# Optimization experiments

Hardware: AMD Instinct MI355X
Metric: run time of the kernel (lower is better)

The kernel has to match this reference:

```python
import jax, jax.numpy as jnp
import numpy as np

N = 256    # b_s == nq == h*q == h*v (forced by the module's reshape/matmul constraints)
A = 1024   # model dim 'a'
K_DIM = 1  # self.k (h*k must equal 1 for the .view to be valid)


def setup_inputs() -> dict:
    key = jax.random.key(0)
    ks = jax.random.split(key, 5)
    s = 0.02
    x = jax.random.normal(ks[0], (N, N, A), dtype=jnp.float32)
    Wq = jax.random.normal(ks[1], (N, A), dtype=jnp.float32) * s      # fc_q: a -> h*q = N
    bq = jnp.zeros((N,), dtype=jnp.float32)
    Wk = jax.random.normal(ks[2], (K_DIM, A), dtype=jnp.float32) * s  # fc_k: a -> h*k = 1
    bk = jnp.zeros((K_DIM,), dtype=jnp.float32)
    Wv = jax.random.normal(ks[3], (N, A), dtype=jnp.float32) * s      # fc_v: a -> h*v = N
    bv = jnp.zeros((N,), dtype=jnp.float32)
    Wo = jax.random.normal(ks[4], (A, N), dtype=jnp.float32) * s      # fc_o: h*v -> a
    bo = jnp.zeros((A,), dtype=jnp.float32)
    return {"x": x, "Wq": Wq, "bq": bq, "Wk": Wk, "bk": bk,
            "Wv": Wv, "bv": bv, "Wo": Wo, "bo": bo}


def reference(x, Wq, bq, Wk, bk, Wv, bv, Wo, bo):
    # q = fc_q(x): (b_s, nq, h*q)
    q = jnp.einsum('bna,qa->bnq', x, Wq) + bq
    # k = fc_k(x).view(b_s, nq).permute(1, 0): (nq, b_s)
    klin = (jnp.einsum('bna,ka->bnk', x, Wk) + bk)[..., 0]  # (b_s, nq)
    kT = klin.T                                             # (nq, b_s)
    # att = matmul(kT, q) / sqrt(self.k): 2D kT broadcast over batch of q
    att = jnp.einsum('nm,bmq->bnq', kT, q) / np.sqrt(np.float32(K_DIM))
    att = jax.nn.softmax(att, axis=-1)  # dropout = identity (eval mode)
    # v = fc_v(x): (b_s, nq, h*v)
    v = jnp.einsum('bna,va->bnv', x, Wv) + bv
    # out = matmul(v, att): batched (nq, h*v) @ (nq, h*q) with h*v == nq
    out = jnp.einsum('bnm,bmq->bnq', v, att)
    # fc_o: (..., h*v) -> (..., a)
    return jnp.einsum('bnv,av->bna', out, Wo) + bo
```

## Files before the change

kernel.cpp:

```cpp
#include <hip/hip_runtime.h>


typedef unsigned short u16;
typedef unsigned int   uint;
using f32x4  = __attribute__((ext_vector_type(4))) float;
using bf16x8 = __attribute__((ext_vector_type(8))) short;
using u16x4  = __attribute__((ext_vector_type(4))) u16;

#define DEVI static __device__ __forceinline__

DEVI u16 f2bf(float f){
  union { float f; uint u; } v; v.f = f;
  uint r = v.u + 0x7fffu + ((v.u >> 16) & 1u);
  return (u16)(r >> 16);
}
DEVI float bf2f(u16 h){
  union { uint u; float f; } v; v.u = ((uint)h) << 16;
  return v.f;
}

typedef const uint __attribute__((address_space(1)))* as1_cuintp;
typedef uint __attribute__((address_space(3)))* as3_uintp;

DEVI void gl_lds16(const void* g, void* l){
  __builtin_amdgcn_global_load_lds((as1_cuintp)g, (as3_uintp)l, 16, 0, 0);
}

template<int ROWS, int NW>
DEVI void stage_tile(const u16* __restrict__ g, long long rowStride,
                     u16* lds, int lane, int wave){
  constexpr int NLD = ROWS >> 3;
  #pragma unroll
  for (int j = 0; j < NLD/NW; ++j){
    int r0  = (wave + NW*j) << 3;
    int row = r0 + (lane >> 3);
    const u16* src = g + (long long)row * rowStride
                       + (((lane & 7) ^ (lane >> 3)) << 3);
    gl_lds16(src, lds + r0 * 64);
  }
}

DEVI bf16x8 ldfrag(const u16* s, int rbase, int kk, int lane){
  int row = rbase + (lane & 15);
  int c   = (kk << 2) + (lane >> 4);
  return *(const bf16x8*)(s + row*64 + ((c ^ (row & 7)) << 3));
}

__global__ __launch_bounds__(512, 2)
void k_qvkl(const float* __restrict__ x,
            const u16* __restrict__ Wqh, const u16* __restrict__ Wql,
            const u16* __restrict__ Wvh,
            const float* __restrict__ Wk, const float* __restrict__ bk,
            const float* __restrict__ bq, const float* __restrict__ bv,
            u16* __restrict__ qTh, u16* __restrict__ qTl,
            u16* __restrict__ vout,
            u16* __restrict__ klTh, u16* __restrict__ klTl)
{
  __shared__ __align__(16) u16 sX [128*64];
  __shared__ __align__(16) u16 sXl[128*64];
  __shared__ __align__(16) u16 sW [2][3*128*64];

  const int tid  = threadIdx.x;
  const int lane = tid & 63;
  const int wave = tid >> 6;
  const int wm   = wave >> 2;
  const int wn   = wave & 3;
  const int tileM = blockIdx.x << 7;

  f32x4 qacc[4][4], vacc[4][4];
  #pragma unroll
  for (int i=0;i<4;i++)
    #pragma unroll
    for (int j=0;j<4;j++){
      qacc[i][j][0]=0.f; qacc[i][j][1]=0.f; qacc[i][j][2]=0.f; qacc[i][j][3]=0.f;
      vacc[i][j][0]=0.f; vacc[i][j][1]=0.f; vacc[i][j][2]=0.f; vacc[i][j][3]=0.f;
    }
  float kacc[4] = {0.f, 0.f, 0.f, 0.f};

  stage_tile<128,8>(Wqh + 0, 1024, sW[0],         lane, wave);
  stage_tile<128,8>(Wql + 0, 1024, sW[0] + 8192,  lane, wave);
  stage_tile<128,8>(Wvh + 0, 1024, sW[0] + 16384, lane, wave);

  for (int kt = 0; kt < 1024; kt += 64){
    #pragma unroll
    for (int h = 0; h < 2; ++h){
      f32x4 xr[4];
      if (h == 0){
        #pragma unroll
        for (int j=0;j<4;j++){
          int f = tid + (j << 9);
          xr[j] = *(const f32x4*)(x + (long long)(tileM + (f >> 4))*1024
                                  + kt + ((f & 15) << 2));
        }
        __builtin_amdgcn_sched_barrier(0);
      }
      const bool last = (kt == 960) && (h == 1);
      if (!last){
        const int nh  = h ^ 1;
        const int nkt = (h == 0) ? kt : kt + 64;
        u16* wb = sW[h ^ 1];
        stage_tile<128,8>(Wqh + (nh << 7)*1024 + nkt, 1024, wb,         lane, wave);
        stage_tile<128,8>(Wql + (nh << 7)*1024 + nkt, 1024, wb + 8192,  lane, wave);
        stage_tile<128,8>(Wvh + (nh << 7)*1024 + nkt, 1024, wb + 16384, lane, wave);
      }
      if (h == 0){
        #pragma unroll
        for (int j=0;j<4;j++){
          int f   = tid + (j << 9);
          int row = f >> 4;
          int c16 = f & 15;
          f32x4 t = xr[j];
          u16x4 h4, l4;
          #pragma unroll
          for (int e=0;e<4;e++){
            u16 hh = f2bf(t[e]);
            h4[e] = hh;
            l4[e] = f2bf(t[e] - bf2f(hh));
          }
          int off = row*64 + (((c16 >> 1) ^ (row & 7)) << 3) + ((c16 & 1) << 2);
          *(u16x4*)(sX  + off) = h4;
          *(u16x4*)(sXl + off) = l4;
          f32x4 w = *(const f32x4*)(Wk + kt + (c16 << 2));
          kacc[j] += t[0]*w[0] + t[1]*w[1] + t[2]*w[2] + t[3]*w[3];
        }
      }
      if (!last) asm volatile("s_waitcnt vmcnt(6) lgkmcnt(0)" ::: "memory");
      else       asm volatile("s_waitcnt vmcnt(0) lgkmcnt(0)" ::: "memory");
      __builtin_amdgcn_s_barrier();
      __builtin_amdgcn_sched_barrier(0);

      {
        const u16* wb = sW[h];
        #pragma unroll
        for (int kk=0;kk<2;kk++){
          bf16x8 a[4], al[4];
          #pragma unroll
          for (int i=0;i<4;i++){
            a[i]  = ldfrag(sX , wm*64 + i*16, kk, lane);
            al[i] = ldfrag(sXl, wm*64 + i*16, kk, lane);
          }
          {
            bf16x8 b[2];
            #pragma unroll
            for (int i=0;i<2;i++) b[i] = ldfrag(wb, wn*32 + i*16, kk, lane);
            #pragma unroll
            for (int mt=0;mt<4;mt++)
              #pragma unroll
              for (int ntl=0;ntl<2;ntl++){
                qacc[mt][(h<<1)|ntl] = __builtin_amdgcn_mfma_f32_16x16x32_bf16(a[mt],  b[ntl], qacc[mt][(h<<1)|ntl], 0,0,0);
                qacc[mt][(h<<1)|ntl] = __builtin_amdgcn_mfma_f32_16x16x32_bf16(al[mt], b[ntl], qacc[mt][(h<<1)|ntl], 0,0,0);
              }
          }
          {
            bf16x8 b[2];
            #pragma unroll
            for (int i=0;i<2;i++) b[i] = ldfrag(wb + 8192, wn*32 + i*16, kk, lane);
            #pragma unroll
            for (int mt=0;mt<4;mt++)
              #pragma unroll
              for (int ntl=0;ntl<2;ntl++)
                qacc[mt][(h<<1)|ntl] = __builtin_amdgcn_mfma_f32_16x16x32_bf16(a[mt], b[ntl], qacc[mt][(h<<1)|ntl], 0,0,0);
          }
          {
            bf16x8 b[2];
            #pragma unroll
            for (int i=0;i<2;i++) b[i] = ldfrag(wb + 16384, wn*32 + i*16, kk, lane);
            #pragma unroll
            for (int mt=0;mt<4;mt++)
              #pragma unroll
              for (int ntl=0;ntl<2;ntl++)
                vacc[mt][(h<<1)|ntl] = __builtin_amdgcn_mfma_f32_16x16x32_bf16(a[mt], b[ntl], vacc[mt][(h<<1)|ntl], 0,0,0);
          }
        }
      }
      asm volatile("s_waitcnt lgkmcnt(0)" ::: "memory");
      __builtin_amdgcn_s_barrier();
      __builtin_amdgcn_sched_barrier(0);
    }
  }

  #pragma unroll
  for (int j=0;j<4;j++){
    #pragma unroll
    for (int m=1;m<16;m<<=1) kacc[j] += __shfl_xor(kacc[j], m, 64);
  }
  if ((lane & 15) == 0){
    #pragma unroll
    for (int j=0;j<4;j++){
      int f = tid + (j << 9);
      int r = tileM + (f >> 4);
      float kv = kacc[j] + bk[0];
      u16 hh = f2bf(kv);
      klTh[(r & 255)*256 + (r >> 8)] = hh;
      klTl[(r & 255)*256 + (r >> 8)] = f2bf(kv - bf2f(hh));
    }
  }

  #pragma unroll
  for (int mt=0;mt<4;mt++)
    #pragma unroll
    for (int ntg=0;ntg<4;ntg++){
      const int gr = tileM + wm*64 + mt*16 + ((lane >> 4) << 2);
      const int gc = ((ntg >> 1) << 7) + wn*32 + ((ntg & 1) << 4) + (lane & 15);
      {
        const int bidx = gr >> 8, m = gr & 255;
        const long long off = ((long long)bidx << 16) + ((long long)gc << 8) + m;
        const float bb = bq[gc];
        u16x4 h4, l4;
        f32x4 v = qacc[mt][ntg];
        #pragma unroll
        for (int r=0;r<4;r++){
          float fq = v[r] + bb;
          u16 hh = f2bf(fq);
          h4[r] = hh;
          l4[r] = f2bf(fq - bf2f(hh));
        }
        *(u16x4*)(qTh + off) = h4;
        *(u16x4*)(qTl + off) = l4;
      }
      {
        const float bb = bv[gc];
        u16* o = vout + (long long)gr * 256 + gc;
        f32x4 v = vacc[mt][ntg];
        #pragma unroll
        for (int r=0;r<4;r++) o[(long long)r * 256] = f2bf(v[r] + bb);
      }
    }
}

template<int WMODE>
__global__ __launch_bounds__(256, 2)
void k_gemm(const u16* __restrict__ Ag,
            const u16* __restrict__ Bhg,
            int N, int K, int tnCount, long long bStrideB,
            const float* __restrict__ bias,
            void* __restrict__ Co)
{
  __shared__ __align__(16) u16 sA[128*64];
  __shared__ __align__(16) u16 sB[128*64];

  const int tid  = threadIdx.x;
  const int lane = tid & 63;
  const int wave = tid >> 6;
  const int wm   = wave >> 1;
  const int wn   = wave & 1;
  const int tn   = blockIdx.x % tnCount;
  const int tm   = blockIdx.x / tnCount;
  const int tileM = tm << 7;
  const int tileN = tn << 7;

  const long long bOff = bStrideB ? (long long)(tileM >> 8) * bStrideB : 0;
  const u16* Bh_t = Bhg + bOff + (long long)tileN * K;

  f32x4 acc[4][4];
  #pragma unroll
  for (int i=0;i<4;i++)
    #pragma unroll
    for (int j=0;j<4;j++){
      acc[i][j][0]=0.f; acc[i][j][1]=0.f; acc[i][j][2]=0.f; acc[i][j][3]=0.f;
    }

  for (int kt = 0; kt < K; kt += 64){
    stage_tile<128,4>(Ag + (long long)tileM * K + kt, K, sA, lane, wave);
    stage_tile<128,4>(Bh_t + kt, K, sB, lane, wave);
    __syncthreads();
    #pragma unroll
    for (int kk=0;kk<2;kk++){
      bf16x8 a[4], b[4];
      #pragma unroll
      for (int i=0;i<4;i++){
        a[i] = ldfrag(sA, wm*64 + i*16, kk, lane);
        b[i] = ldfrag(sB, wn*64 + i*16, kk, lane);
      }
      #pragma unroll
      for (int mt=0;mt<4;mt++)
        #pragma unroll
        for (int nt=0;nt<4;nt++)
          acc[mt][nt] = __builtin_amdgcn_mfma_f32_16x16x32_bf16(a[mt], b[nt], acc[mt][nt], 0,0,0);
    }
    __syncthreads();
  }

  #pragma unroll
  for (int mt=0;mt<4;mt++)
    #pragma unroll
    for (int nt=0;nt<4;nt++){
      const int gr = tileM + wm*64 + mt*16 + ((lane >> 4) << 2);
      const int gc = tileN + wn*64 + nt*16 + (lane & 15);
      const float bb = bias ? bias[gc] : 0.f;
      f32x4 v = acc[mt][nt];
      if (WMODE == 0){
        float* o = (float*)Co + (long long)gr * N + gc;
        #pragma unroll
        for (int r=0;r<4;r++) o[(long long)r * N] = v[r] + bb;
      } else {
        u16* o = (u16*)Co + (long long)gr * N + gc;
        #pragma unroll
        for (int r=0;r<4;r++) o[(long long)r * N] = f2bf(v[r] + bb);
      }
    }
}

__global__ __launch_bounds__(256, 1)
void k_logits(const u16* __restrict__ qTh, const u16* __restrict__ qTl,
              const u16* __restrict__ klTh, const u16* __restrict__ klTl,
              u16* __restrict__ attT)
{
  __shared__ __align__(16) union U {
    struct S { u16 Ah[64*64]; u16 Al[64*64]; u16 Bh[256*64]; u16 Bl[256*64]; } s;
    float L[64*260];
  } u;
  __shared__ float rmax[64], rinv[64];

  const int tid  = threadIdx.x;
  const int lane = tid & 63;
  const int wave = tid >> 6;
  const int bidx  = blockIdx.x >> 2;
  const int ntile = blockIdx.x & 3;

  f32x4 acc[4][4];
  #pragma unroll
  for (int i=0;i<4;i++)
    #pragma unroll
    for (int j=0;j<4;j++){
      acc[i][j][0]=0.f; acc[i][j][1]=0.f; acc[i][j][2]=0.f; acc[i][j][3]=0.f;
    }

  for (int kt=0; kt<256; kt+=64){
    stage_tile<64,4> (klTh + (ntile << 6)*256 + kt, 256, u.s.Ah, lane, wave);
    stage_tile<64,4> (klTl + (ntile << 6)*256 + kt, 256, u.s.Al, lane, wave);
    stage_tile<256,4>(qTh + ((long long)bidx << 16) + kt, 256, u.s.Bh, lane, wave);
    stage_tile<256,4>(qTl + ((long long)bidx << 16) + kt, 256, u.s.Bl, lane, wave);
    __syncthreads();
    #pragma unroll
    for (int kk=0;kk<2;kk++){
      bf16x8 a[4], al[4], b[4], bl[4];
      #pragma unroll
      for (int i=0;i<4;i++){
        a[i]  = ldfrag(u.s.Ah, i*16, kk, lane);
        al[i] = ldfrag(u.s.Al, i*16, kk, lane);
        b[i]  = ldfrag(u.s.Bh, wave*64 + i*16, kk, lane);
        bl[i] = ldfrag(u.s.Bl, wave*64 + i*16, kk, lane);
      }
      #pragma unroll
      for (int mt=0;mt<4;mt++)
        #pragma unroll
        for (int nt=0;nt<4;nt++){
          acc[mt][nt] = __builtin_amdgcn_mfma_f32_16x16x32_bf16(a[mt],  b[nt],  acc[mt][nt], 0,0,0);
          acc[mt][nt] = __builtin_amdgcn_mfma_f32_16x16x32_bf16(al[mt], b[nt],  acc[mt][nt], 0,0,0);
          acc[mt][nt] = __builtin_amdgcn_mfma_f32_16x16x32_bf16(a[mt],  bl[nt], acc[mt][nt], 0,0,0);
        }
    }
    __syncthreads();
  }

  #pragma unroll
  for (int mt=0;mt<4;mt++)
    #pragma unroll
    for (int nt=0;nt<4;nt++){
      const int r0 = mt*16 + ((lane >> 4) << 2);
      const int c  = wave*64 + nt*16 + (lane & 15);
      #pragma unroll
      for (int r=0;r<4;r++) u.L[(r0 + r)*260 + c] = acc[mt][nt][r];
    }
  __syncthreads();

  {
    const int row = tid >> 2, sub = tid & 3;
    const float* Lr = &u.L[row*260 + sub*64];
    float mx = -3.4e38f;
    for (int i=0;i<64;i++) mx = fmaxf(mx, Lr[i]);
    mx = fmaxf(mx, __shfl_xor(mx, 1, 64));
    mx = fmaxf(mx, __shfl_xor(mx, 2, 64));
    float s = 0.f;
    for (int i=0;i<64;i++) s += __expf(Lr[i] - mx);
    s += __shfl_xor(s, 1, 64);
    s += __shfl_xor(s, 2, 64);
    if (sub == 0){ rmax[row] = mx; rinv[row] = 1.f / s; }
  }
  __syncthreads();

  {
    const int qq = tid;
    u16* dst = attT + ((long long)bidx << 16) + qq*256 + (ntile << 6);
    #pragma unroll
    for (int n0=0;n0<64;n0+=8){
      bf16x8 pk;
      #pragma unroll
      for (int e=0;e<8;e++){
        int n = n0 + e;
        float v = __expf(u.L[n*260 + qq] - rmax[n]) * rinv[n];
        pk[e] = (short)f2bf(v);
      }
      *(bf16x8*)(dst + n0) = pk;
    }
  }
}

__global__ void k_split(const float* __restrict__ w, u16* __restrict__ hi,
                        u16* __restrict__ lo, int n4){
  int i = blockIdx.x * blockDim.x + threadIdx.x;
  if (i >= n4) return;
  f32x4 v = ((const f32x4*)w)[i];
  u16x4 h, l;
  #pragma unroll
  for (int e=0;e<4;e++){
    u16 hh = f2bf(v[e]);
    h[e] = hh;
    l[e] = f2bf(v[e] - bf2f(hh));
  }
  ((u16x4*)hi)[i] = h;
  ((u16x4*)lo)[i] = l;
}

extern "C" void kernel_launch(void* const* d_in, const int* in_sizes, int n_in,
                              void* d_out, int out_size, void* d_ws, size_t ws_size,
                              hipStream_t stream){
  (void)in_sizes; (void)n_in; (void)out_size; (void)ws_size;
  const float* x  = (const float*)d_in[0];
  const float* Wq = (const float*)d_in[1];
  const float* bq = (const float*)d_in[2];
  const float* Wk = (const float*)d_in[3];
  const float* bk = (const float*)d_in[4];
  const float* Wv = (const float*)d_in[5];
  const float* bv = (const float*)d_in[6];
  const float* Wo = (const float*)d_in[7];
  const float* bo = (const float*)d_in[8];

  char* ob = (char*)d_out;
  u16* qTh  = (u16*)(ob);
  u16* qTl  = (u16*)(ob + (size_t)33554432);
  u16* vh   = (u16*)(ob + (size_t)67108864);
  u16* attT = (u16*)(ob + (size_t)100663296);
  char* wb = (char*)d_ws;
  u16* omh  = (u16*)(wb);
  u16* Wqh  = (u16*)(wb + (size_t)33554432);
  u16* Wql  = Wqh + 262144;
  u16* Wvh  = Wql + 262144;
  u16* Wvl  = Wvh + 262144;
  u16* Woh  = Wvl + 262144;
  u16* Wol  = Woh + 262144;
  u16* klTh = Wol + 262144;
  u16* klTl = klTh + 65536;

  k_split<<<256, 256, 0, stream>>>(Wq, Wqh, Wql, 65536);
  k_split<<<256, 256, 0, stream>>>(Wv, Wvh, Wvl, 65536);
  k_split<<<256, 256, 0, stream>>>(Wo, Woh, Wol, 65536);

  k_qvkl<<<512, 512, 0, stream>>>(x, Wqh, Wql, Wvh, Wk, bk, bq, bv,
                                  qTh, qTl, vh, klTh, klTl);
  k_logits<<<1024, 256, 0, stream>>>(qTh, qTl, klTh, klTl, attT);
  k_gemm<1><<<1024, 256, 0, stream>>>(vh, attT, 256, 256, 2, 65536, nullptr, omh);
  k_gemm<0><<<4096, 256, 0, stream>>>(omh, Woh, 1024, 256, 8, 0, bo, d_out);
}
```

Baseline: 370.0 us.

## Stage x tiles asynchronously into LDS and single-buffer weight tiles

The fused Q/V/K projection kernel now prefetches the fp32 x tile for the next k-step straight into a double-buffered LDS region with global_load_lds, rather than loading it through registers. The bf16 hi/lo split and the Wk dot product then read from LDS, and Wk is cached in shared memory once. To free LDS for this, the weight tiles drop from double to single buffering, and each half-step reloads them after a barrier. The aim is to hide x global-load latency and cut register pressure, but weight-load latency is now mostly exposed before each MFMA phase.

```diff
diff --git a/kernel.cpp b/kernel.cpp
--- a/kernel.cpp
+++ b/kernel.cpp
@@ -37,6 +37,17 @@
     const u16* src = g + (long long)row * rowStride
                        + (((lane & 7) ^ (lane >> 3)) << 3);
     gl_lds16(src, lds + r0 * 64);
+  }
+}
+
+DEVI void stage_xf(const float* __restrict__ x, int tileM, int kt,
+                   float* dst, int lane, int wave){
+  #pragma unroll
+  for (int j=0;j<4;j++){
+    int r0 = (wave + 8*j) << 2;
+    const float* src = x + (long long)(tileM + r0 + (lane >> 4))*1024
+                         + kt + ((lane & 15) << 2);
+    gl_lds16(src, dst + r0*64);
   }
 }
 
@@ -56,9 +67,12 @@
             u16* __restrict__ vout,
             u16* __restrict__ klTh, u16* __restrict__ klTl)
 {
-  __shared__ __align__(16) u16 sX [128*64];
-  __shared__ __align__(16) u16 sXl[128*64];
-  __shared__ __align__(16) u16 sW [2][3*128*64];
+  __shared__ __align__(16) float sXF0[128*64];
+  __shared__ __align__(16) float sXF1[128*64];
+  __shared__ __align__(16) float sWk [1024];
+  __shared__ __align__(16) u16   sX  [128*64];
+  __shared__ __align__(16) u16   sXl [128*64];
+  __shared__ __align__(16) u16   sW  [3*128*64];
 
   const int tid  = threadIdx.x;
   const int lane = tid & 63;
@@ -77,106 +91,144 @@
     }
   float kacc[4] = {0.f, 0.f, 0.f, 0.f};
 
-  stage_tile<128,8>(Wqh + 0, 1024, sW[0],         lane, wave);
-  stage_tile<128,8>(Wql + 0, 1024, sW[0] + 8192,  lane, wave);
-  stage_tile<128,8>(Wvh + 0, 1024, sW[0] + 16384, lane, wave);
+  sWk[tid]       = Wk[tid];
+  sWk[tid + 512] = Wk[tid + 512];
+  __builtin_amdgcn_sched_barrier(0);
+  stage_xf(x, tileM, 0, sXF0, lane, wave);
 
   for (int kt = 0; kt < 1024; kt += 64){
-    #pragma unroll
-    for (int h = 0; h < 2; ++h){
-      f32x4 xr[4];
-      if (h == 0){
-        #pragma unroll
-        for (int j=0;j<4;j++){
-          int f = tid + (j << 9);
-          xr[j] = *(const f32x4*)(x + (long long)(tileM + (f >> 4))*1024
-                                  + kt + ((f & 15) << 2));
-        }
-        __builtin_amdgcn_sched_barrier(0);
-      }
-      const bool last = (kt == 960) && (h == 1);
-      if (!last){
-        const int nh  = h ^ 1;
-        const int nkt = (h == 0) ? kt : kt + 64;
-        u16* wb = sW[h ^ 1];
-        stage_tile<128,8>(Wqh + (nh << 7)*1024 + nkt, 1024, wb,         lane, wave);
-        stage_tile<128,8>(Wql + (nh << 7)*1024 + nkt, 1024, wb + 8192,  lane, wave);
-        stage_tile<128,8>(Wvh + (nh << 7)*1024 + nkt, 1024, wb + 16384, lane, wave);
-      }
-      if (h == 0){
-        #pragma unroll
-        for (int j=0;j<4;j++){
-          int f   = tid + (j << 9);
-          int row = f >> 4;
-          int c16 = f & 15;
-          f32x4 t = xr[j];
-          u16x4 h4, l4;
+    float* xfCur = (kt & 64) ? sXF1 : sXF0;
+    float* xfNxt = (kt & 64) ? sXF0 : sXF1;
+    const bool lastKt = (kt == 960);
+
+    stage_tile<128,8>(Wqh + kt, 1024, sW,         lane, wave);
+    stage_tile<128,8>(Wql + kt, 1024, sW + 8192,  lane, wave);
+    stage_tile<128,8>(Wvh + kt, 1024, sW + 16384, lane, wave);
+    asm volatile("s_waitcnt vmcnt(6) lgkmcnt(0)" ::: "memory");
+    __builtin_amdgcn_s_barrier();
+    __builtin_amdgcn_sched_barrier(0);
+
+    #pragma unroll
+    for (int j=0;j<4;j++){
+      int f   = tid + (j << 9);
+      int row = f >> 4;
+      int c16 = f & 15;
+      f32x4 t = *(const f32x4*)(xfCur + row*64 + (c16 << 2));
+      u16x4 h4, l4;
+      #pragma unroll
+      for (int e=0;e<4;e++){
+        u16 hh = f2bf(t[e]);
+        h4[e] = hh;
+        l4[e] = f2bf(t[e] - bf2f(hh));
+      }
+      int off = row*64 + (((c16 >> 1) ^ (row & 7)) << 3) + ((c16 & 1) << 2);
+      *(u16x4*)(sX  + off) = h4;
+      *(u16x4*)(sXl + off) = l4;
+      f32x4 w = *(const f32x4*)(sWk + kt + (c16 << 2));
+      kacc[j] += t[0]*w[0] + t[1]*w[1] + t[2]*w[2] + t[3]*w[3];
+    }
+    asm volatile("s_waitcnt vmcnt(0) lgkmcnt(0)" ::: "memory");
+    __builtin_amdgcn_s_barrier();
+    __builtin_amdgcn_sched_barrier(0);
+
+    #pragma unroll
+    for (int kk=0;kk<2;kk++){
+      bf16x8 a[4], al[4];
+      #pragma unroll
+      for (int i=0;i<4;i++){
+        a[i]  = ldfrag(sX , wm*64 + i*16, kk, lane);
+        al[i] = ldfrag(sXl, wm*64 + i*16, kk, lane);
+      }
+      {
+        bf16x8 b[2];
+        #pragma unroll
+        for (int i=0;i<2;i++) b[i] = ldfrag(sW, wn*32 + i*16, kk, lane);
+        #pragma unroll
+        for (int mt=0;mt<4;mt++)
           #pragma unroll
-          for (int e=0;e<4;e++){
-            u16 hh = f2bf(t[e]);
-            h4[e] = hh;
-            l4[e] = f2bf(t[e] - bf2f(hh));
+          for (int ntl=0;ntl<2;ntl++){
+            qacc[mt][ntl] = __builtin_amdgcn_mfma_f32_16x16x32_bf16(a[mt],  b[ntl], qacc[mt][ntl], 0,0,0);
+            qacc[mt][ntl] = __builtin_amdgcn_mfma_f32_16x16x32_bf16(al[mt], b[ntl], qacc[mt][ntl], 0,0,0);
           }
-          int off = row*64 + (((c16 >> 1) ^ (row & 7)) << 3) + ((c16 & 1) << 2);
-          *(u16x4*)(sX  + off) = h4;
-          *(u16x4*)(sXl + off) = l4;
-          f32x4 w = *(const f32x4*)(Wk + kt + (c16 << 2));
-          kacc[j] += t[0]*w[0] + t[1]*w[1] + t[2]*w[2] + t[3]*w[3];
-        }
-      }
-      if (!last) asm volatile("s_waitcnt vmcnt(6) lgkmcnt(0)" ::: "memory");
-      else       asm volatile("s_waitcnt vmcnt(0) lgkmcnt(0)" ::: "memory");
-      __builtin_amdgcn_s_barrier();
-      __builtin_amdgcn_sched_barrier(0);
-
-      {
-        const u16* wb = sW[h];
-        #pragma unroll
-        for (int kk=0;kk<2;kk++){
-          bf16x8 a[4], al[4];
+      }
+      {
+        bf16x8 b[2];
+        #pragma unroll
+        for (int i=0;i<2;i++) b[i] = ldfrag(sW + 8192, wn*32 + i*16, kk, lane);
+        #pragma unroll
+        for (int mt=0;mt<4;mt++)
           #pragma unroll
-          for (int i=0;i<4;i++){
-            a[i]  = ldfrag(sX , wm*64 + i*16, kk, lane);
-            al[i] = ldfrag(sXl, wm*64 + i*16, kk, lane);
+          for (int ntl=0;ntl<2;ntl++)
+            qacc[mt][ntl] = __builtin_amdgcn_mfma_f32_16x16x32_bf16(a[mt], b[ntl], qacc[mt][ntl], 0,0,0);
+      }
+      {
+        bf16x8 b[2];
+        #pragma unroll
+        for (int i=0;i<2;i++) b[i] = ldfrag(sW + 16384, wn*32 + i*16, kk, lane);
+        #pragma unroll
+        for (int mt=0;mt<4;mt++)
+          #pragma unroll
+          for (int ntl=0;ntl<2;ntl++)
+            vacc[mt][ntl] = __builtin_amdgcn_mfma_f32_16x16x32_bf16(a[mt], b[ntl], vacc[mt][ntl], 0,0,0);
+      }
+    }
+    asm volatile("s_waitcnt lgkmcnt(0)" ::: "memory");
+    __builtin_amdgcn_s_barrier();
+    __builtin_amdgcn_sched_barrier(0);
+
+    stage_tile<128,8>(Wqh + 131072 + kt, 1024, sW,         lane, wave);
+    stage_tile<128,8>(Wql + 131072 + kt, 1024, sW + 8192,  lane, wave);
+    stage_tile<128,8>(Wvh + 131072 + kt, 1024, sW + 16384, lane, wave);
+    if (!lastKt) stage_xf(x, tileM, kt + 64, xfNxt, lane, wave);
+    if (!lastKt) asm volatile("s_waitcnt vmcnt(4) lgkmcnt(0)" ::: "memory");
+    else         asm volatile("s_waitcnt vmcnt(0) lgkmcnt(0)" ::: "memory");
+    __builtin_amdgcn_s_barrier();
+    __builtin_amdgcn_sched_barrier(0);
+
+    #pragma unroll
+    for (int kk=0;kk<2;kk++){
+      bf16x8 a[4], al[4];
+      #pragma unroll
+      for (int i=0;i<4;i++){
+        a[i]  = ldfrag(sX , wm*64 + i*16, kk, lane);
+        al[i] = ldfrag(sXl, wm*64 + i*16, kk, lane);
+      }
+      {
+        bf16x8 b[2];
+        #pragma unroll
+        for (int i=0;i<2;i++) b[i] = ldfrag(sW, wn*32 + i*16, kk, lane);
+        #pragma unroll
+        for (int mt=0;mt<4;mt++)
+          #pragma unroll
+          for (int ntl=0;ntl<2;ntl++){
+            qacc[mt][2|ntl] = __builtin_amdgcn_mfma_f32_16x16x32_bf16(a[mt],  b[ntl], qacc[mt][2|ntl], 0,0,0);
+            qacc[mt][2|ntl] = __builtin_amdgcn_mfma_f32_16x16x32_bf16(al[mt], b[ntl], qacc[mt][2|ntl], 0,0,0);
           }
-          {
-            bf16x8 b[2];
-            #pragma unroll
-            for (int i=0;i<2;i++) b[i] = ldfrag(wb, wn*32 + i*16, kk, lane);
-            #pragma unroll
-            for (int mt=0;mt<4;mt++)
-              #pragma unroll
-              for (int ntl=0;ntl<2;ntl++){
-                qacc[mt][(h<<1)|ntl] = __builtin_amdgcn_mfma_f32_16x16x32_bf16(a[mt],  b[ntl], qacc[mt][(h<<1)|ntl], 0,0,0);
-                qacc[mt][(h<<1)|ntl] = __builtin_amdgcn_mfma_f32_16x16x32_bf16(al[mt], b[ntl], qacc[mt][(h<<1)|ntl], 0,0,0);
-              }
-          }
-          {
-            bf16x8 b[2];
-            #pragma unroll
-            for (int i=0;i<2;i++) b[i] = ldfrag(wb + 8192, wn*32 + i*16, kk, lane);
-            #pragma unroll
-            for (int mt=0;mt<4;mt++)
-              #pragma unroll
-              for (int ntl=0;ntl<2;ntl++)
-                qacc[mt][(h<<1)|ntl] = __builtin_amdgcn_mfma_f32_16x16x32_bf16(a[mt], b[ntl], qacc[mt][(h<<1)|ntl], 0,0,0);
-          }
-          {
-            bf16x8 b[2];
-            #pragma unroll
-            for (int i=0;i<2;i++) b[i] = ldfrag(wb + 16384, wn*32 + i*16, kk, lane);
-            #pragma unroll
-            for (int mt=0;mt<4;mt++)
-              #pragma unroll
-              for (int ntl=0;ntl<2;ntl++)
-                vacc[mt][(h<<1)|ntl] = __builtin_amdgcn_mfma_f32_16x16x32_bf16(a[mt], b[ntl], vacc[mt][(h<<1)|ntl], 0,0,0);
-          }
-        }
-      }
-      asm volatile("s_waitcnt lgkmcnt(0)" ::: "memory");
-      __builtin_amdgcn_s_barrier();
-      __builtin_amdgcn_sched_barrier(0);
-    }
+      }
+      {
+        bf16x8 b[2];
+        #pragma unroll
+        for (int i=0;i<2;i++) b[i] = ldfrag(sW + 8192, wn*32 + i*16, kk, lane);
+        #pragma unroll
+        for (int mt=0;mt<4;mt++)
+          #pragma unroll
+          for (int ntl=0;ntl<2;ntl++)
+            qacc[mt][2|ntl] = __builtin_amdgcn_mfma_f32_16x16x32_bf16(a[mt], b[ntl], qacc[mt][2|ntl], 0,0,0);
+      }
+      {
+        bf16x8 b[2];
+        #pragma unroll
+        for (int i=0;i<2;i++) b[i] = ldfrag(sW + 16384, wn*32 + i*16, kk, lane);
+        #pragma unroll
+        for (int mt=0;mt<4;mt++)
+          #pragma unroll
+          for (int ntl=0;ntl<2;ntl++)
+            vacc[mt][2|ntl] = __builtin_amdgcn_mfma_f32_16x16x32_bf16(a[mt], b[ntl], vacc[mt][2|ntl], 0,0,0);
+      }
+    }
+    asm volatile("s_waitcnt lgkmcnt(0)" ::: "memory");
+    __builtin_amdgcn_s_barrier();
+    __builtin_amdgcn_sched_barrier(0);
   }
 
   #pragma unroll
```

New measurement: 383.7 us. +3.7%, slower.
